# Optimization experiments

Measured on AMD Instinct MI355X. Metric: run time of the kernel, lower is better.

## Reference

```python
import jax, jax.numpy as jnp
import numpy as np

D_MODEL, D_K, D_V, H, M = 512, 64, 64, 8, 40
LN_EPS = 1e-3  # keras LayerNormalization default epsilon


def setup_inputs() -> dict:
    key = jax.random.key(0)
    ks = jax.random.split(key, 12)
    b, nq, nk = 16, 1024, 1024
    s = 1.0 / np.sqrt(D_MODEL)
    return {
        "queries": jax.random.normal(ks[0], (b, nq, D_MODEL), jnp.float32),
        "keys": jax.random.normal(ks[1], (b, nk, D_MODEL), jnp.float32),
        "values": jax.random.normal(ks[2], (b, nk, D_MODEL), jnp.float32),
        "attention_weights": jax.random.uniform(ks[3], (b, 1, nq, nk), jnp.float32),
        "Wq": jax.random.normal(ks[4], (D_MODEL, H * D_K), jnp.float32) * s,
        "bq": jnp.zeros((H * D_K,), jnp.float32),
        "Wk": jax.random.normal(ks[5], (D_MODEL, H * D_K), jnp.float32) * s,
        "bk": jnp.zeros((H * D_K,), jnp.float32),
        "Wv": jax.random.normal(ks[6], (D_MODEL, H * D_V), jnp.float32) * s,
        "bv": jnp.zeros((H * D_V,), jnp.float32),
        "Wo": jax.random.normal(ks[7], (H * D_V, D_MODEL), jnp.float32) * (1.0 / np.sqrt(H * D_V)),
        "bo": jnp.zeros((D_MODEL,), jnp.float32),
        "memK": jax.random.normal(ks[8], (1, M, H * D_K), jnp.float32) * (1.0 / D_K),
        "memV": jax.random.normal(ks[9], (1, M, H * D_V), jnp.float32) * (1.0 / M),
        "gamma": jnp.ones((D_MODEL,), jnp.float32),
        "beta": jnp.zeros((D_MODEL,), jnp.float32),
    }


def reference(queries, keys, values, attention_weights, Wq, bq, Wk, bk, Wv, bv,
              Wo, bo, memK, memV, gamma, beta):
    b, nq, _ = queries.shape
    nk = keys.shape[1]
    # scaled learned memory slots
    mem_k = np.sqrt(D_K).astype(np.float32) * memK      # [1, M, H*D_K]
    mem_v = np.sqrt(M).astype(np.float32) * memV        # [1, M, H*D_V]
    # projections
    q = (queries @ Wq + bq).reshape(b, nq, H, D_K).transpose(0, 2, 1, 3)   # [b,h,nq,dk]
    k_proj = keys @ Wk + bk                                                # [b,nk,H*D_K]
    v_proj = values @ Wv + bv                                              # [b,nk,H*D_V]
    k_cat = jnp.concatenate([k_proj, jnp.broadcast_to(mem_k, (b, M, H * D_K))], axis=1)
    v_cat = jnp.concatenate([v_proj, jnp.broadcast_to(mem_v, (b, M, H * D_V))], axis=1)
    k = k_cat.reshape(b, nk + M, H, D_K).transpose(0, 2, 1, 3)             # [b,h,nk+m,dk]
    v = v_cat.reshape(b, nk + M, H, D_V).transpose(0, 2, 1, 3)             # [b,h,nk+m,dv]
    att = jnp.einsum('bhqd,bhkd->bhqk', q, k) / np.sqrt(D_K).astype(np.float32)
    # only the non-memory columns are modulated by attention_weights
    att = jnp.concatenate([att[..., :nk] * attention_weights, att[..., nk:]], axis=-1)
    att = jax.nn.softmax(att, axis=-1)
    out = jnp.einsum('bhqk,bhkd->bhqd', att, v).transpose(0, 2, 1, 3).reshape(b, nq, H * D_V)
    out = out @ Wo + bo  # dropout is identity at inference
    # residual + LayerNorm (keras eps=1e-3)
    x = queries + out
    mu = jnp.mean(x, axis=-1, keepdims=True)
    var = jnp.mean((x - mu) ** 2, axis=-1, keepdims=True)
    return gamma * (x - mu) * jax.lax.rsqrt(var + LN_EPS) + beta
```

## Files before the change

### kernel.cpp

```cpp
#include <hip/hip_runtime.h>
#include <hip/hip_bf16.h>
#include <math.h>

typedef __attribute__((ext_vector_type(8))) short bf16x8;
typedef __attribute__((ext_vector_type(4))) short s16x4;
typedef __attribute__((ext_vector_type(4))) float f32x4;

static __device__ __forceinline__ short f2bf(float f) {
    union { float f; unsigned u; } v; v.f = f;
    unsigned r = v.u + 0x7FFFu + ((v.u >> 16) & 1u);
    return (short)(r >> 16);
}

#define GL2LDS16(g, s) __builtin_amdgcn_global_load_lds( \
    (const __attribute__((address_space(1))) void*)(g),  \
    (__attribute__((address_space(3))) void*)(s), 16, 0, 0)

__global__ __launch_bounds__(256) void wt_kernel(
    const float* __restrict__ Wq, const float* __restrict__ Wk,
    const float* __restrict__ Wv, const float* __restrict__ Wo,
    short* __restrict__ WqT, short* __restrict__ WkT,
    short* __restrict__ WvT, short* __restrict__ WoT)
{
    __shared__ short lds[64][65];
    const float* src; short* dst;
    if (blockIdx.z == 0)      { src = Wq; dst = WqT; }
    else if (blockIdx.z == 1) { src = Wk; dst = WkT; }
    else if (blockIdx.z == 2) { src = Wv; dst = WvT; }
    else                      { src = Wo; dst = WoT; }
    const int kb = blockIdx.x * 64, nb = blockIdx.y * 64;
    const int t = threadIdx.x;
    const int c = t & 63, r0 = t >> 6;
#pragma unroll
    for (int rr = 0; rr < 16; ++rr) {
        const int r = r0 * 16 + rr;
        lds[c][r] = f2bf(src[(size_t)(kb + r) * 512 + nb + c]);
    }
    __syncthreads();
#pragma unroll
    for (int rr = 0; rr < 16; ++rr) {
        const int n = r0 * 16 + rr;
        dst[(size_t)(nb + n) * 512 + kb + c] = lds[n][c];
    }
}

__global__ __launch_bounds__(256) void mem_kernel(
    const float* __restrict__ memK, const float* __restrict__ memV,
    short* __restrict__ Kb, short* __restrict__ VbT)
{
    const int idx = blockIdx.x * 256 + threadIdx.x;
    if (idx >= 16 * 8 * 40 * 64) return;
    {
        const int d = idx & 63;
        const int m = (idx >> 6) % 40;
        const int h = (idx / 2560) & 7;
        const int b = idx / 20480;
        Kb[(((size_t)(b * 8 + h)) * 1064 + 1024 + m) * 64 + d] =
            f2bf(8.0f * memK[m * 512 + h * 64 + d]);
    }
    {
        const int m = idx % 40;
        const int d = (idx / 40) & 63;
        const int h = (idx / 2560) & 7;
        const int b = idx / 20480;
        VbT[(((size_t)(b * 8 + h)) * 64 + d) * 1088 + 1024 + m] =
            f2bf(sqrtf(40.0f) * memV[m * 512 + h * 64 + d]);
    }
}

__global__ __launch_bounds__(256) void proj_gemm(
    const float* __restrict__ Aq, const float* __restrict__ Ak, const float* __restrict__ Av,
    const short* __restrict__ WqT, const short* __restrict__ WkT, const short* __restrict__ WvT,
    const float* __restrict__ bq, const float* __restrict__ bk, const float* __restrict__ bv,
    short* __restrict__ Qb, short* __restrict__ Kb, short* __restrict__ VbT)
{
    __shared__ float As[128 * 64];
    __shared__ short Bs[128 * 64];

    const float* A; const short* BT; const float* bias; short* out;
    int vmode, OUTROWS;
    if (blockIdx.y == 0)      { A = Aq; BT = WqT; bias = bq; out = Qb;  vmode = 0; OUTROWS = 1024; }
    else if (blockIdx.y == 1) { A = Ak; BT = WkT; bias = bk; out = Kb;  vmode = 0; OUTROWS = 1064; }
    else                      { A = Av; BT = WvT; bias = bv; out = VbT; vmode = 1; OUTROWS = 1064; }

    const int id = blockIdx.x;
    const int mt = (id & 7) + 8 * (id >> 5);
    const int nt = (id >> 3) & 3;
    const int m0 = mt * 128, n0 = nt * 128;

    const int t = threadIdx.x;
    const int lane = t & 63, w = t >> 6;
    const int wr = w >> 1, wc = w & 1;
    const int l16 = lane & 15, g4 = lane >> 4;

    f32x4 acc[4][4];
#pragma unroll
    for (int i = 0; i < 4; ++i)
#pragma unroll
        for (int j = 0; j < 4; ++j) acc[i][j] = (f32x4){0.f, 0.f, 0.f, 0.f};

    const char* Asb = reinterpret_cast<const char*>(As);
    const char* Bsb = reinterpret_cast<const char*>(Bs);

    for (int kt = 0; kt < 8; ++kt) {
        const int k0 = kt * 64;
#pragma unroll
        for (int p = 0; p < 8; ++p) {
            const int row = p * 16 + (t >> 4);
            const int ck = (t & 15) ^ (row & 7);
            GL2LDS16(&A[(size_t)(m0 + row) * 512 + k0 + ck * 4],
                     (char*)As + (p * 256 + t) * 16);
        }
#pragma unroll
        for (int p = 0; p < 4; ++p) {
            const int row = p * 32 + (t >> 3);
            const int ck = (t & 7) ^ (row & 7);
            GL2LDS16(&BT[(size_t)(n0 + row) * 512 + k0 + ck * 8],
                     (char*)Bs + (p * 256 + t) * 16);
        }
        __syncthreads();
#pragma unroll
        for (int kk = 0; kk < 2; ++kk) {
            bf16x8 af[4], bfr[4];
#pragma unroll
            for (int mi = 0; mi < 4; ++mi) {
                const int row = wr * 64 + mi * 16 + l16;
                const int c0 = (kk * 8 + g4 * 2) ^ (row & 7);
                const int c1 = (kk * 8 + g4 * 2 + 1) ^ (row & 7);
                const float4 f0 = *reinterpret_cast<const float4*>(Asb + row * 256 + c0 * 16);
                const float4 f1 = *reinterpret_cast<const float4*>(Asb + row * 256 + c1 * 16);
                bf16x8 a;
                a[0] = f2bf(f0.x); a[1] = f2bf(f0.y); a[2] = f2bf(f0.z); a[3] = f2bf(f0.w);
                a[4] = f2bf(f1.x); a[5] = f2bf(f1.y); a[6] = f2bf(f1.z); a[7] = f2bf(f1.w);
                af[mi] = a;
            }
#pragma unroll
            for (int ni = 0; ni < 4; ++ni) {
                const int row = wc * 64 + ni * 16 + l16;
                const int ck = (kk * 4 + g4) ^ (row & 7);
                bfr[ni] = *reinterpret_cast<const bf16x8*>(Bsb + row * 128 + ck * 16);
            }
            __builtin_amdgcn_s_setprio(1);
#pragma unroll
            for (int mi = 0; mi < 4; ++mi)
#pragma unroll
                for (int ni = 0; ni < 4; ++ni)
                    acc[mi][ni] = __builtin_amdgcn_mfma_f32_16x16x32_bf16(af[mi], bfr[ni], acc[mi][ni], 0, 0, 0);
            __builtin_amdgcn_s_setprio(0);
        }
        __syncthreads();
    }
#pragma unroll
    for (int mi = 0; mi < 4; ++mi) {
#pragma unroll
        for (int ni = 0; ni < 4; ++ni) {
            const int col = n0 + wc * 64 + ni * 16 + l16;
            const int h = col >> 6, d = col & 63;
            const float bb = bias[col];
#pragma unroll
            for (int r = 0; r < 4; ++r) {
                const int rowg = m0 + wr * 64 + mi * 16 + g4 * 4 + r;
                const int b = rowg >> 10, nn = rowg & 1023;
                const short val = f2bf(acc[mi][ni][r] + bb);
                if (vmode)
                    out[(((size_t)b * 8 + h) * 64 + d) * 1088 + nn] = val;
                else
                    out[(((size_t)b * 8 + h) * OUTROWS + nn) * 64 + d] = val;
            }
        }
    }
}

__global__ __launch_bounds__(256) void attn_kernel(
    const short* __restrict__ Qb, const short* __restrict__ Kb,
    const short* __restrict__ VbT, const float* __restrict__ aw,
    short* __restrict__ AO)
{
    __shared__ short Ks[64][72];
    __shared__ short Vs[64][72];
    __shared__ short Ps[4][16][72];

    const int n = blockIdx.x;
    const int xcd = n & 7, s_ = n >> 3, j = s_ & 7, gh = s_ >> 3;
    const int g = gh * 8 + xcd;
    const int h = j, qt = g & 15, b = g >> 4;
    const int bh = b * 8 + h;
    const int t = threadIdx.x;
    const int lane = t & 63, w = t >> 6;
    const int l16 = lane & 15, g4 = lane >> 4;
    const int qrow0 = qt * 64 + w * 16;

    bf16x8 qf0, qf1;
    {
        const short* qp = Qb + ((size_t)bh * 1024 + qrow0 + l16) * 64 + g4 * 8;
        qf0 = *reinterpret_cast<const bf16x8*>(qp);
        qf1 = *reinterpret_cast<const bf16x8*>(qp + 32);
    }

    f32x4 O[4];
#pragma unroll
    for (int i = 0; i < 4; ++i) O[i] = (f32x4){0.f, 0.f, 0.f, 0.f};
    float m_r[4] = {-1e30f, -1e30f, -1e30f, -1e30f};
    float l_r[4] = {0.f, 0.f, 0.f, 0.f};

    const int str = t >> 2;
    const int stc = (t & 3) * 16;

    for (int kt = 0; kt < 17; ++kt) {
        const int kb = kt * 64;
        const bool useaw = (kb < 1024);
        float awv[4][4];
        if (useaw) {
#pragma unroll
            for (int r = 0; r < 4; ++r) {
                const size_t awbase = ((size_t)b * 1024 + qrow0 + g4 * 4 + r) * 1024 + kb + l16;
#pragma unroll
                for (int sub = 0; sub < 4; ++sub)
                    awv[r][sub] = aw[awbase + sub * 16];
            }
        }
        {
            const int rg = kb + str;
            bf16x8 k0 = {0,0,0,0,0,0,0,0}, k1 = {0,0,0,0,0,0,0,0};
            if (rg < 1064) {
                const short* kp = &Kb[((size_t)bh * 1064 + rg) * 64 + stc];
                k0 = *reinterpret_cast<const bf16x8*>(kp);
                k1 = *reinterpret_cast<const bf16x8*>(kp + 8);
            }
            *reinterpret_cast<bf16x8*>(&Ks[str][stc]) = k0;
            *reinterpret_cast<bf16x8*>(&Ks[str][stc + 8]) = k1;
        }
        {
            const short* vp = &VbT[((size_t)bh * 64 + str) * 1088 + kb + stc];
            bf16x8 v0 = {0,0,0,0,0,0,0,0}, v1 = {0,0,0,0,0,0,0,0};
            if (kb + stc + 8 <= 1064)  v0 = *reinterpret_cast<const bf16x8*>(vp);
            if (kb + stc + 16 <= 1064) v1 = *reinterpret_cast<const bf16x8*>(vp + 8);
            *reinterpret_cast<bf16x8*>(&Vs[str][stc]) = v0;
            *reinterpret_cast<bf16x8*>(&Vs[str][stc + 8]) = v1;
        }
        __syncthreads();

        f32x4 S[4];
        __builtin_amdgcn_s_setprio(1);
#pragma unroll
        for (int sub = 0; sub < 4; ++sub) {
            bf16x8 kf0 = *reinterpret_cast<const bf16x8*>(&Ks[sub * 16 + l16][g4 * 8]);
            bf16x8 kf1 = *reinterpret_cast<const bf16x8*>(&Ks[sub * 16 + l16][32 + g4 * 8]);
            f32x4 z = {0.f, 0.f, 0.f, 0.f};
            z = __builtin_amdgcn_mfma_f32_16x16x32_bf16(qf0, kf0, z, 0, 0, 0);
            S[sub] = __builtin_amdgcn_mfma_f32_16x16x32_bf16(qf1, kf1, z, 0, 0, 0);
        }
        __builtin_amdgcn_s_setprio(0);

        const bool tail = (kb + 64 > 1064);
        float sv[4][4], mx[4];
#pragma unroll
        for (int r = 0; r < 4; ++r) {
#pragma unroll
            for (int sub = 0; sub < 4; ++sub) {
                float x = S[sub][r] * 0.125f;
                if (useaw) x *= awv[r][sub];
                if (tail && (kb + sub * 16 + l16 >= 1064)) x = -1e30f;
                sv[r][sub] = x;
            }
            float m2 = fmaxf(fmaxf(sv[r][0], sv[r][1]), fmaxf(sv[r][2], sv[r][3]));
#pragma unroll
            for (int off = 1; off < 16; off <<= 1)
                m2 = fmaxf(m2, __shfl_xor(m2, off));
            mx[r] = m2;
        }
        bool grew = false;
#pragma unroll
        for (int r = 0; r < 4; ++r) grew = grew || (mx[r] > m_r[r] + 8.0f);
        if (__any(grew)) {
#pragma unroll
            for (int r = 0; r < 4; ++r) {
                const float mn = fmaxf(m_r[r], mx[r]);
                const float corr = __expf(m_r[r] - mn);
                m_r[r] = mn;
                l_r[r] *= corr;
#pragma unroll
                for (int i = 0; i < 4; ++i) O[i][r] *= corr;
            }
        }
#pragma unroll
        for (int r = 0; r < 4; ++r) {
            float rs = 0.f;
#pragma unroll
            for (int sub = 0; sub < 4; ++sub) {
                const float p = __expf(sv[r][sub] - m_r[r]);
                rs += p;
                Ps[w][g4 * 4 + r][sub * 16 + l16] = f2bf(p);
            }
#pragma unroll
            for (int off = 1; off < 16; off <<= 1)
                rs += __shfl_xor(rs, off);
            l_r[r] += rs;
        }
        bf16x8 pf0 = *reinterpret_cast<const bf16x8*>(&Ps[w][l16][g4 * 8]);
        bf16x8 pf1 = *reinterpret_cast<const bf16x8*>(&Ps[w][l16][32 + g4 * 8]);
        __builtin_amdgcn_s_setprio(1);
#pragma unroll
        for (int sub = 0; sub < 4; ++sub) {
            bf16x8 vf0 = *reinterpret_cast<const bf16x8*>(&Vs[sub * 16 + l16][g4 * 8]);
            bf16x8 vf1 = *reinterpret_cast<const bf16x8*>(&Vs[sub * 16 + l16][32 + g4 * 8]);
            O[sub] = __builtin_amdgcn_mfma_f32_16x16x32_bf16(pf0, vf0, O[sub], 0, 0, 0);
            O[sub] = __builtin_amdgcn_mfma_f32_16x16x32_bf16(pf1, vf1, O[sub], 0, 0, 0);
        }
        __builtin_amdgcn_s_setprio(0);
        __syncthreads();
    }
#pragma unroll
    for (int r = 0; r < 4; ++r) {
        const float inv = 1.0f / l_r[r];
        const int qg = qrow0 + g4 * 4 + r;
        const size_t base = ((size_t)b * 1024 + qg) * 512 + h * 64;
#pragma unroll
        for (int sub = 0; sub < 4; ++sub)
            AO[base + sub * 16 + l16] = f2bf(O[sub][r] * inv);
    }
}

__global__ __launch_bounds__(256) void out_gemm(
    const short* __restrict__ A, const short* __restrict__ BT,
    const float* __restrict__ bias, const float* __restrict__ resid,
    float* __restrict__ out)
{
    __shared__ short Asm[128 * 64];
    __shared__ short Bs[128 * 64];

    const int id = blockIdx.x;
    const int mt = (id & 7) + 8 * (id >> 5);
    const int nt = (id >> 3) & 3;
    const int m0 = mt * 128, n0 = nt * 128;

    const int t = threadIdx.x;
    const int lane = t & 63, w = t >> 6;
    const int wr = w >> 1, wc = w & 1;
    const int l16 = lane & 15, g4 = lane >> 4;

    f32x4 acc[4][4];
#pragma unroll
    for (int i = 0; i < 4; ++i)
#pragma unroll
        for (int j = 0; j < 4; ++j) acc[i][j] = (f32x4){0.f, 0.f, 0.f, 0.f};

    const char* Asb = reinterpret_cast<const char*>(Asm);
    const char* Bsb = reinterpret_cast<const char*>(Bs);

    for (int kt = 0; kt < 8; ++kt) {
        const int k0 = kt * 64;
#pragma unroll
        for (int p = 0; p < 4; ++p) {
            const int row = p * 32 + (t >> 3);
            const int ck = (t & 7) ^ (row & 7);
            GL2LDS16(&A[(size_t)(m0 + row) * 512 + k0 + ck * 8],
                     (char*)Asm + (p * 256 + t) * 16);
            GL2LDS16(&BT[(size_t)(n0 + row) * 512 + k0 + ck * 8],
                     (char*)Bs + (p * 256 + t) * 16);
        }
        __syncthreads();
#pragma unroll
        for (int kk = 0; kk < 2; ++kk) {
            bf16x8 af[4], bfr[4];
#pragma unroll
            for (int mi = 0; mi < 4; ++mi) {
                const int row = wr * 64 + mi * 16 + l16;
                const int ck = (kk * 4 + g4) ^ (row & 7);
                af[mi] = *reinterpret_cast<const bf16x8*>(Asb + row * 128 + ck * 16);
            }
#pragma unroll
            for (int ni = 0; ni < 4; ++ni) {
                const int row = wc * 64 + ni * 16 + l16;
                const int ck = (kk * 4 + g4) ^ (row & 7);
                bfr[ni] = *reinterpret_cast<const bf16x8*>(Bsb + row * 128 + ck * 16);
            }
            __builtin_amdgcn_s_setprio(1);
#pragma unroll
            for (int mi = 0; mi < 4; ++mi)
#pragma unroll
                for (int ni = 0; ni < 4; ++ni)
                    acc[mi][ni] = __builtin_amdgcn_mfma_f32_16x16x32_bf16(af[mi], bfr[ni], acc[mi][ni], 0, 0, 0);
            __builtin_amdgcn_s_setprio(0);
        }
        __syncthreads();
    }
#pragma unroll
    for (int mi = 0; mi < 4; ++mi) {
#pragma unroll
        for (int ni = 0; ni < 4; ++ni) {
            const int col = n0 + wc * 64 + ni * 16 + l16;
            const float bb = bias[col];
#pragma unroll
            for (int r = 0; r < 4; ++r) {
                const int rowg = m0 + wr * 64 + mi * 16 + g4 * 4 + r;
                out[(size_t)rowg * 512 + col] = acc[mi][ni][r] + bb + resid[(size_t)rowg * 512 + col];
            }
        }
    }
}

__global__ __launch_bounds__(256) void ln_kernel(
    float* __restrict__ x, const float* __restrict__ gamma, const float* __restrict__ beta)
{
    const int row = blockIdx.x * 4 + (threadIdx.x >> 6);
    const int lane = threadIdx.x & 63;
    float* rp = x + (size_t)row * 512;
    const float4 v0 = *reinterpret_cast<const float4*>(&rp[lane * 4]);
    const float4 v1 = *reinterpret_cast<const float4*>(&rp[256 + lane * 4]);
    float s = v0.x + v0.y + v0.z + v0.w + v1.x + v1.y + v1.z + v1.w;
    float sq = v0.x * v0.x + v0.y * v0.y + v0.z * v0.z + v0.w * v0.w
             + v1.x * v1.x + v1.y * v1.y + v1.z * v1.z + v1.w * v1.w;
#pragma unroll
    for (int off = 1; off < 64; off <<= 1) {
        s += __shfl_xor(s, off);
        sq += __shfl_xor(sq, off);
    }
    const float mu = s * (1.f / 512.f);
    const float var = sq * (1.f / 512.f) - mu * mu;
    const float inv = rsqrtf(var + 1e-3f);
    const float4 g0 = *reinterpret_cast<const float4*>(&gamma[lane * 4]);
    const float4 g1 = *reinterpret_cast<const float4*>(&gamma[256 + lane * 4]);
    const float4 b0 = *reinterpret_cast<const float4*>(&beta[lane * 4]);
    const float4 b1 = *reinterpret_cast<const float4*>(&beta[256 + lane * 4]);
    float4 o0, o1;
    o0.x = (v0.x - mu) * inv * g0.x + b0.x;
    o0.y = (v0.y - mu) * inv * g0.y + b0.y;
    o0.z = (v0.z - mu) * inv * g0.z + b0.z;
    o0.w = (v0.w - mu) * inv * g0.w + b0.w;
    o1.x = (v1.x - mu) * inv * g1.x + b1.x;
    o1.y = (v1.y - mu) * inv * g1.y + b1.y;
    o1.z = (v1.z - mu) * inv * g1.z + b1.z;
    o1.w = (v1.w - mu) * inv * g1.w + b1.w;
    *reinterpret_cast<float4*>(&rp[lane * 4]) = o0;
    *reinterpret_cast<float4*>(&rp[256 + lane * 4]) = o1;
}

extern "C" void kernel_launch(void* const* d_in, const int* in_sizes, int n_in,
                              void* d_out, int out_size, void* d_ws, size_t ws_size,
                              hipStream_t stream) {
    const float* queries = (const float*)d_in[0];
    const float* keys    = (const float*)d_in[1];
    const float* values  = (const float*)d_in[2];
    const float* aw      = (const float*)d_in[3];
    const float* Wq = (const float*)d_in[4];
    const float* bq = (const float*)d_in[5];
    const float* Wk = (const float*)d_in[6];
    const float* bk = (const float*)d_in[7];
    const float* Wv = (const float*)d_in[8];
    const float* bv = (const float*)d_in[9];
    const float* Wo = (const float*)d_in[10];
    const float* bo = (const float*)d_in[11];
    const float* memK = (const float*)d_in[12];
    const float* memV = (const float*)d_in[13];
    const float* gamma = (const float*)d_in[14];
    const float* beta  = (const float*)d_in[15];
    float* out = (float*)d_out;

    char* ws = (char*)d_ws;
    short* WqT = (short*)(ws + 0);
    short* WkT = (short*)(ws + 524288);
    short* WvT = (short*)(ws + 1048576);
    short* WoT = (short*)(ws + 1572864);
    short* Qb  = (short*)(ws + 2097152);
    short* Kb  = (short*)(ws + 2097152 + 16777216);
    short* VbT = (short*)(ws + 2097152 + 16777216 + 17432576);
    short* AO  = (short*)(ws + 2097152 + 16777216 + 17432576 + 17825792);

    wt_kernel<<<dim3(8, 8, 4), 256, 0, stream>>>(Wq, Wk, Wv, Wo, WqT, WkT, WvT, WoT);
    mem_kernel<<<dim3(1280), 256, 0, stream>>>(memK, memV, Kb, VbT);
    proj_gemm<<<dim3(512, 3), 256, 0, stream>>>(queries, keys, values,
                                                WqT, WkT, WvT, bq, bk, bv,
                                                Qb, Kb, VbT);
    attn_kernel<<<dim3(2048), 256, 0, stream>>>(Qb, Kb, VbT, aw, AO);
    out_gemm<<<dim3(512), 256, 0, stream>>>(AO, WoT, bo, queries, out);
    ln_kernel<<<dim3(4096), 256, 0, stream>>>(out, gamma, beta);
}
```

Before: 392.5 us.

## Double-buffer GEMM K loops, use exp2 softmax with packed bf16 conversion

```diff
diff --git a/kernel.cpp b/kernel.cpp
--- a/kernel.cpp
+++ b/kernel.cpp
@@ -10,6 +10,22 @@
     union { float f; unsigned u; } v; v.f = f;
     unsigned r = v.u + 0x7FFFu + ((v.u >> 16) & 1u);
     return (short)(r >> 16);
+}
+
+static __device__ __forceinline__ unsigned cvtpk(float a, float b) {
+    unsigned r;
+    asm("v_cvt_pk_bf16_f32 %0, %1, %2" : "=v"(r) : "v"(a), "v"(b));
+    return r;
+}
+static __device__ __forceinline__ float fexp2(float x) {
+    float r;
+    asm("v_exp_f32 %0, %1" : "=v"(r) : "v"(x));
+    return r;
+}
+static __device__ __forceinline__ bf16x8 pack4(unsigned u0, unsigned u1, unsigned u2, unsigned u3) {
+    union { unsigned u[4]; bf16x8 v; } x;
+    x.u[0] = u0; x.u[1] = u1; x.u[2] = u2; x.u[3] = u3;
+    return x.v;
 }
 
 #define GL2LDS16(g, s) __builtin_amdgcn_global_load_lds( \
@@ -63,7 +79,8 @@
         const int d = (idx / 40) & 63;
         const int h = (idx / 2560) & 7;
         const int b = idx / 20480;
-        VbT[(((size_t)(b * 8 + h)) * 64 + d) * 1088 + 1024 + m] =
+        const int pos = 1024 + ((m & 15) << 2) + (m >> 4);
+        VbT[(((size_t)(b * 8 + h)) * 64 + d) * 1088 + pos] =
             f2bf(sqrtf(40.0f) * memV[m * 512 + h * 64 + d]);
     }
 }
@@ -74,8 +91,8 @@
     const float* __restrict__ bq, const float* __restrict__ bk, const float* __restrict__ bv,
     short* __restrict__ Qb, short* __restrict__ Kb, short* __restrict__ VbT)
 {
-    __shared__ float As[128 * 64];
-    __shared__ short Bs[128 * 64];
+    __shared__ float As[2][4096];
+    __shared__ short Bs[2][4096];
 
     const float* A; const short* BT; const float* bias; short* out;
     int vmode, OUTROWS;
@@ -99,57 +116,60 @@
 #pragma unroll
         for (int j = 0; j < 4; ++j) acc[i][j] = (f32x4){0.f, 0.f, 0.f, 0.f};
 
-    const char* Asb = reinterpret_cast<const char*>(As);
-    const char* Bsb = reinterpret_cast<const char*>(Bs);
-
-    for (int kt = 0; kt < 8; ++kt) {
-        const int k0 = kt * 64;
-#pragma unroll
-        for (int p = 0; p < 8; ++p) {
-            const int row = p * 16 + (t >> 4);
-            const int ck = (t & 15) ^ (row & 7);
-            GL2LDS16(&A[(size_t)(m0 + row) * 512 + k0 + ck * 4],
-                     (char*)As + (p * 256 + t) * 16);
-        }
-#pragma unroll
-        for (int p = 0; p < 4; ++p) {
-            const int row = p * 32 + (t >> 3);
-            const int ck = (t & 7) ^ (row & 7);
-            GL2LDS16(&BT[(size_t)(n0 + row) * 512 + k0 + ck * 8],
-                     (char*)Bs + (p * 256 + t) * 16);
-        }
+#define STAGE_P(kt_, buf_) {                                                   \
+    const int k0_ = (kt_) * 32;                                                \
+    _Pragma("unroll")                                                          \
+    for (int p = 0; p < 4; ++p) {                                              \
+        const int row = p * 32 + (t >> 3);                                     \
+        const int ck = (t & 7) ^ (row & 7);                                    \
+        GL2LDS16(&A[(size_t)(m0 + row) * 512 + k0_ + ck * 4],                  \
+                 &As[buf_][(p * 256 + t) * 4]);                                \
+    }                                                                          \
+    _Pragma("unroll")                                                          \
+    for (int p = 0; p < 2; ++p) {                                              \
+        const int row = p * 64 + (t >> 2);                                     \
+        const int ck = (t & 3) ^ (row & 3);                                    \
+        GL2LDS16(&BT[(size_t)(n0 + row) * 512 + k0_ + ck * 8],                 \
+                 &Bs[buf_][(p * 256 + t) * 8]);                                \
+    } }
+
+    int cur = 0;
+    STAGE_P(0, 0);
+    __syncthreads();
+
+    for (int kt = 0; kt < 16; ++kt) {
+        if (kt < 15) STAGE_P(kt + 1, cur ^ 1);
+        const char* Ab = (const char*)As[cur];
+        const char* Bb = (const char*)Bs[cur];
+        bf16x8 af[4], bfr[4];
+#pragma unroll
+        for (int mi = 0; mi < 4; ++mi) {
+            const int row = wr * 64 + mi * 16 + l16;
+            const int c0 = (g4 * 2) ^ (row & 7);
+            const int c1 = (g4 * 2 + 1) ^ (row & 7);
+            const float4 f0 = *reinterpret_cast<const float4*>(Ab + row * 128 + c0 * 16);
+            const float4 f1 = *reinterpret_cast<const float4*>(Ab + row * 128 + c1 * 16);
+            af[mi] = pack4(cvtpk(f0.x, f0.y), cvtpk(f0.z, f0.w),
+                           cvtpk(f1.x, f1.y), cvtpk(f1.z, f1.w));
+        }
+#pragma unroll
+        for (int ni = 0; ni < 4; ++ni) {
+            const int row = wc * 64 + ni * 16 + l16;
+            const int ck = g4 ^ (row & 3);
+            bfr[ni] = *reinterpret_cast<const bf16x8*>(Bb + row * 64 + ck * 16);
+        }
+        __builtin_amdgcn_s_setprio(1);
+#pragma unroll
+        for (int mi = 0; mi < 4; ++mi)
+#pragma unroll
+            for (int ni = 0; ni < 4; ++ni)
+                acc[mi][ni] = __builtin_amdgcn_mfma_f32_16x16x32_bf16(af[mi], bfr[ni], acc[mi][ni], 0, 0, 0);
+        __builtin_amdgcn_s_setprio(0);
         __syncthreads();
-#pragma unroll
-        for (int kk = 0; kk < 2; ++kk) {
-            bf16x8 af[4], bfr[4];
-#pragma unroll
-            for (int mi = 0; mi < 4; ++mi) {
-                const int row = wr * 64 + mi * 16 + l16;
-                const int c0 = (kk * 8 + g4 * 2) ^ (row & 7);
-                const int c1 = (kk * 8 + g4 * 2 + 1) ^ (row & 7);
-                const float4 f0 = *reinterpret_cast<const float4*>(Asb + row * 256 + c0 * 16);
-                const float4 f1 = *reinterpret_cast<const float4*>(Asb + row * 256 + c1 * 16);
-                bf16x8 a;
-                a[0] = f2bf(f0.x); a[1] = f2bf(f0.y); a[2] = f2bf(f0.z); a[3] = f2bf(f0.w);
-                a[4] = f2bf(f1.x); a[5] = f2bf(f1.y); a[6] = f2bf(f1.z); a[7] = f2bf(f1.w);
-                af[mi] = a;
-            }
-#pragma unroll
-            for (int ni = 0; ni < 4; ++ni) {
-                const int row = wc * 64 + ni * 16 + l16;
-                const int ck = (kk * 4 + g4) ^ (row & 7);
-                bfr[ni] = *reinterpret_cast<const bf16x8*>(Bsb + row * 128 + ck * 16);
-            }
-            __builtin_amdgcn_s_setprio(1);
-#pragma unroll
-            for (int mi = 0; mi < 4; ++mi)
-#pragma unroll
-                for (int ni = 0; ni < 4; ++ni)
-                    acc[mi][ni] = __builtin_amdgcn_mfma_f32_16x16x32_bf16(af[mi], bfr[ni], acc[mi][ni], 0, 0, 0);
-            __builtin_amdgcn_s_setprio(0);
-        }
-        __syncthreads();
-    }
+        cur ^= 1;
+    }
+#undef STAGE_P
+
 #pragma unroll
     for (int mi = 0; mi < 4; ++mi) {
 #pragma unroll
@@ -162,10 +182,13 @@
                 const int rowg = m0 + wr * 64 + mi * 16 + g4 * 4 + r;
                 const int b = rowg >> 10, nn = rowg & 1023;
                 const short val = f2bf(acc[mi][ni][r] + bb);
-                if (vmode)
-                    out[(((size_t)b * 8 + h) * 64 + d) * 1088 + nn] = val;
-                else
+                if (vmode) {
+                    const int w6 = nn & 63;
+                    const int pos = (nn & ~63) + ((w6 & 15) << 2) + (w6 >> 4);
+                    out[(((size_t)b * 8 + h) * 64 + d) * 1088 + pos] = val;
+                } else {
                     out[(((size_t)b * 8 + h) * OUTROWS + nn) * 64 + d] = val;
+                }
             }
         }
     }
@@ -189,6 +212,7 @@
     const int lane = t & 63, w = t >> 6;
     const int l16 = lane & 15, g4 = lane >> 4;
     const int qrow0 = qt * 64 + w * 16;
+    const float C = 0.1803368801f;
 
     bf16x8 qf0, qf1;
     {
@@ -200,8 +224,8 @@
     f32x4 O[4];
 #pragma unroll
     for (int i = 0; i < 4; ++i) O[i] = (f32x4){0.f, 0.f, 0.f, 0.f};
-    float m_r[4] = {-1e30f, -1e30f, -1e30f, -1e30f};
-    float l_r[4] = {0.f, 0.f, 0.f, 0.f};
+    float M2 = -1e30f;
+    float l_p[4] = {0.f, 0.f, 0.f, 0.f};
 
     const int str = t >> 2;
     const int stc = (t & 3) * 16;
@@ -209,34 +233,25 @@
     for (int kt = 0; kt < 17; ++kt) {
         const int kb = kt * 64;
         const bool useaw = (kb < 1024);
-        float awv[4][4];
+        float awc[4][4];
         if (useaw) {
 #pragma unroll
             for (int r = 0; r < 4; ++r) {
                 const size_t awbase = ((size_t)b * 1024 + qrow0 + g4 * 4 + r) * 1024 + kb + l16;
 #pragma unroll
                 for (int sub = 0; sub < 4; ++sub)
-                    awv[r][sub] = aw[awbase + sub * 16];
+                    awc[r][sub] = aw[awbase + sub * 16] * C;
             }
         }
         {
-            const int rg = kb + str;
-            bf16x8 k0 = {0,0,0,0,0,0,0,0}, k1 = {0,0,0,0,0,0,0,0};
-            if (rg < 1064) {
-                const short* kp = &Kb[((size_t)bh * 1064 + rg) * 64 + stc];
-                k0 = *reinterpret_cast<const bf16x8*>(kp);
-                k1 = *reinterpret_cast<const bf16x8*>(kp + 8);
-            }
-            *reinterpret_cast<bf16x8*>(&Ks[str][stc]) = k0;
-            *reinterpret_cast<bf16x8*>(&Ks[str][stc + 8]) = k1;
+            const short* kp = &Kb[((size_t)bh * 1064 + kb + str) * 64 + stc];
+            *reinterpret_cast<bf16x8*>(&Ks[str][stc]) = *reinterpret_cast<const bf16x8*>(kp);
+            *reinterpret_cast<bf16x8*>(&Ks[str][stc + 8]) = *reinterpret_cast<const bf16x8*>(kp + 8);
         }
         {
             const short* vp = &VbT[((size_t)bh * 64 + str) * 1088 + kb + stc];
-            bf16x8 v0 = {0,0,0,0,0,0,0,0}, v1 = {0,0,0,0,0,0,0,0};
-            if (kb + stc + 8 <= 1064)  v0 = *reinterpret_cast<const bf16x8*>(vp);
-            if (kb + stc + 16 <= 1064) v1 = *reinterpret_cast<const bf16x8*>(vp + 8);
-            *reinterpret_cast<bf16x8*>(&Vs[str][stc]) = v0;
-            *reinterpret_cast<bf16x8*>(&Vs[str][stc + 8]) = v1;
+            *reinterpret_cast<bf16x8*>(&Vs[str][stc]) = *reinterpret_cast<const bf16x8*>(vp);
+            *reinterpret_cast<bf16x8*>(&Vs[str][stc + 8]) = *reinterpret_cast<const bf16x8*>(vp + 8);
         }
         __syncthreads();
 
@@ -253,49 +268,42 @@
         __builtin_amdgcn_s_setprio(0);
 
         const bool tail = (kb + 64 > 1064);
-        float sv[4][4], mx[4];
+        float sv[4][4];
+        float pm = -1e30f;
 #pragma unroll
         for (int r = 0; r < 4; ++r) {
 #pragma unroll
             for (int sub = 0; sub < 4; ++sub) {
-                float x = S[sub][r] * 0.125f;
-                if (useaw) x *= awv[r][sub];
+                float x = S[sub][r] * (useaw ? awc[r][sub] : C);
                 if (tail && (kb + sub * 16 + l16 >= 1064)) x = -1e30f;
                 sv[r][sub] = x;
+                pm = fmaxf(pm, x);
             }
-            float m2 = fmaxf(fmaxf(sv[r][0], sv[r][1]), fmaxf(sv[r][2], sv[r][3]));
-#pragma unroll
-            for (int off = 1; off < 16; off <<= 1)
-                m2 = fmaxf(m2, __shfl_xor(m2, off));
-            mx[r] = m2;
-        }
-        bool grew = false;
-#pragma unroll
-        for (int r = 0; r < 4; ++r) grew = grew || (mx[r] > m_r[r] + 8.0f);
-        if (__any(grew)) {
-#pragma unroll
-            for (int r = 0; r < 4; ++r) {
-                const float mn = fmaxf(m_r[r], mx[r]);
-                const float corr = __expf(m_r[r] - mn);
-                m_r[r] = mn;
-                l_r[r] *= corr;
-#pragma unroll
-                for (int i = 0; i < 4; ++i) O[i][r] *= corr;
-            }
+        }
+#pragma unroll
+        for (int off = 1; off < 64; off <<= 1)
+            pm = fmaxf(pm, __shfl_xor(pm, off));
+        if (__any(pm > M2 + 8.0f)) {
+            const float corr = fexp2(M2 - pm);
+            M2 = pm;
+#pragma unroll
+            for (int r = 0; r < 4; ++r) l_p[r] *= corr;
+#pragma unroll
+            for (int i = 0; i < 4; ++i)
+#pragma unroll
+                for (int r = 0; r < 4; ++r) O[i][r] *= corr;
         }
 #pragma unroll
         for (int r = 0; r < 4; ++r) {
-            float rs = 0.f;
-#pragma unroll
-            for (int sub = 0; sub < 4; ++sub) {
-                const float p = __expf(sv[r][sub] - m_r[r]);
-                rs += p;
-                Ps[w][g4 * 4 + r][sub * 16 + l16] = f2bf(p);
-            }
-#pragma unroll
-            for (int off = 1; off < 16; off <<= 1)
-                rs += __shfl_xor(rs, off);
-            l_r[r] += rs;
+            const float p0 = fexp2(sv[r][0] - M2);
+            const float p1 = fexp2(sv[r][1] - M2);
+            const float p2 = fexp2(sv[r][2] - M2);
+            const float p3 = fexp2(sv[r][3] - M2);
+            l_p[r] += (p0 + p1) + (p2 + p3);
+            int2 pk;
+            pk.x = (int)cvtpk(p0, p1);
+            pk.y = (int)cvtpk(p2, p3);
+            *reinterpret_cast<int2*>(&Ps[w][g4 * 4 + r][l16 * 4]) = pk;
         }
         bf16x8 pf0 = *reinterpret_cast<const bf16x8*>(&Ps[w][l16][g4 * 8]);
         bf16x8 pf1 = *reinterpret_cast<const bf16x8*>(&Ps[w][l16][32 + g4 * 8]);
@@ -312,7 +320,13 @@
     }
 #pragma unroll
     for (int r = 0; r < 4; ++r) {
-        const float inv = 1.0f / l_r[r];
+#pragma unroll
+        for (int off = 1; off < 16; off <<= 1)
+            l_p[r] += __shfl_xor(l_p[r], off);
+    }
+#pragma unroll
+    for (int r = 0; r < 4; ++r) {
+        const float inv = 1.0f / l_p[r];
         const int qg = qrow0 + g4 * 4 + r;
         const size_t base = ((size_t)b * 1024 + qg) * 512 + h * 64;
 #pragma unroll
@@ -326,8 +340,8 @@
     const float* __restrict__ bias, const float* __restrict__ resid,
     float* __restrict__ out)
 {
-    __shared__ short Asm[128 * 64];
-    __shared__ short Bs[128 * 64];
+    __shared__ short Asm[2][4096];
+    __shared__ short Bs[2][4096];
 
     const int id = blockIdx.x;
     const int mt = (id & 7) + 8 * (id >> 5);
@@ -345,46 +359,51 @@
 #pragma unroll
         for (int j = 0; j < 4; ++j) acc[i][j] = (f32x4){0.f, 0.f, 0.f, 0.f};
 
-    const char* Asb = reinterpret_cast<const char*>(Asm);
-    const char* Bsb = reinterpret_cast<const char*>(Bs);
-
-    for (int kt = 0; kt < 8; ++kt) {
-        const int k0 = kt * 64;
-#pragma unroll
-        for (int p = 0; p < 4; ++p) {
-            const int row = p * 32 + (t >> 3);
-            const int ck = (t & 7) ^ (row & 7);
-            GL2LDS16(&A[(size_t)(m0 + row) * 512 + k0 + ck * 8],
-                     (char*)Asm + (p * 256 + t) * 16);
-            GL2LDS16(&BT[(size_t)(n0 + row) * 512 + k0 + ck * 8],
-                     (char*)Bs + (p * 256 + t) * 16);
-        }
+#define STAGE_O(kt_, buf_) {                                                   \
+    const int k0_ = (kt_) * 32;                                                \
+    _Pragma("unroll")                                                          \
+    for (int p = 0; p < 2; ++p) {                                              \
+        const int row = p * 64 + (t >> 2);                                     \
+        const int ck = (t & 3) ^ (row & 3);                                    \
+        GL2LDS16(&A[(size_t)(m0 + row) * 512 + k0_ + ck * 8],                  \
+                 &Asm[buf_][(p * 256 + t) * 8]);                               \
+        GL2LDS16(&BT[(size_t)(n0 + row) * 512 + k0_ + ck * 8],                 \
+                 &Bs[buf_][(p * 256 + t) * 8]);                                \
+    } }
+
+    int cur = 0;
+    STAGE_O(0, 0);
+    __syncthreads();
+
+    for (int kt = 0; kt < 16; ++kt) {
+        if (kt < 15) STAGE_O(kt + 1, cur ^ 1);
+        const char* Ab = (const char*)Asm[cur];
+        const char* Bb = (const char*)Bs[cur];
+        bf16x8 af[4], bfr[4];
+#pragma unroll
+        for (int mi = 0; mi < 4; ++mi) {
+            const int row = wr * 64 + mi * 16 + l16;
+            const int ck = g4 ^ (row & 3);
+            af[mi] = *reinterpret_cast<const bf16x8*>(Ab + row * 64 + ck * 16);
+        }
+#pragma unroll
+        for (int ni = 0; ni < 4; ++ni) {
+            const int row = wc * 64 + ni * 16 + l16;
+            const int ck = g4 ^ (row & 3);
+            bfr[ni] = *reinterpret_cast<const bf16x8*>(Bb + row * 64 + ck * 16);
+        }
+        __builtin_amdgcn_s_setprio(1);
+#pragma unroll
+        for (int mi = 0; mi < 4; ++mi)
+#pragma unroll
+            for (int ni = 0; ni < 4; ++ni)
+                acc[mi][ni] = __builtin_amdgcn_mfma_f32_16x16x32_bf16(af[mi], bfr[ni], acc[mi][ni], 0, 0, 0);
+        __builtin_amdgcn_s_setprio(0);
         __syncthreads();
-#pragma unroll
-        for (int kk = 0; kk < 2; ++kk) {
-            bf16x8 af[4], bfr[4];
-#pragma unroll
-            for (int mi = 0; mi < 4; ++mi) {
-                const int row = wr * 64 + mi * 16 + l16;
-                const int ck = (kk * 4 + g4) ^ (row & 7);
-                af[mi] = *reinterpret_cast<const bf16x8*>(Asb + row * 128 + ck * 16);
-            }
-#pragma unroll
-            for (int ni = 0; ni < 4; ++ni) {
-                const int row = wc * 64 + ni * 16 + l16;
-                const int ck = (kk * 4 + g4) ^ (row & 7);
-                bfr[ni] = *reinterpret_cast<const bf16x8*>(Bsb + row * 128 + ck * 16);
-            }
-            __builtin_amdgcn_s_setprio(1);
-#pragma unroll
-            for (int mi = 0; mi < 4; ++mi)
-#pragma unroll
-                for (int ni = 0; ni < 4; ++ni)
-                    acc[mi][ni] = __builtin_amdgcn_mfma_f32_16x16x32_bf16(af[mi], bfr[ni], acc[mi][ni], 0, 0, 0);
-            __builtin_amdgcn_s_setprio(0);
-        }
-        __syncthreads();
-    }
+        cur ^= 1;
+    }
+#undef STAGE_O
+
 #pragma unroll
     for (int mi = 0; mi < 4; ++mi) {
 #pragma unroll
```

Result: no change. 398.3 us (+1.5%).
